# Kernel tuning notes

Measured on AMD Instinct MI355X. Metric: run time of the kernel, lower is better.

Reference implementation:

```python
import jax, jax.numpy as jnp
import numpy as np

# Pyramid configuration (mirrors InstancePyramid: init level grid + requested levels)
INIT_SIZE = (200, 200)
LEVEL_SIZES = [(200, 200), (100, 100), (50, 50), (25, 25), (13, 13)]
G = 28            # shared gaussian table side = feature_scale(7) * 4
CTR = 13          # table center index = 7*2 - 1
N_INST = 512


def _gaussian_table():
    # exp(-ln2 * ((x-13)^2 + (y-13)^2) / 7^2), identical to shared_gaussian_masks()
    xs = jnp.arange(G, dtype=jnp.float32)
    d2 = (xs - CTR) ** 2
    return jnp.exp(-jnp.log(jnp.float32(2.0)) * (d2[:, None] + d2[None, :]) / jnp.float32(7 ** 2))


def setup_inputs() -> dict:
    key = jax.random.key(0)
    pos = jax.random.randint(key, (N_INST, 2), 0, INIT_SIZE[0], dtype=jnp.int32)
    shared_mask = _gaussian_table()  # the fixed learnable-free 28x28 gaussian crop source
    return {"pos": pos, "shared_mask": shared_mask}


def _level_masks(shared_mask, pos, level_size):
    # Vectorized form of get_feature_gaussian_mask over all instances.
    H, W = level_size
    H0, W0 = INIT_SIZE
    # get_root_level_pos: round(pos / init_size * req_size)
    lh = jnp.round(pos[:, 0].astype(jnp.float32) / H0 * H).astype(jnp.int32)  # [N]
    lw = jnp.round(pos[:, 1].astype(jnp.float32) / W0 * W).astype(jnp.int32)  # [N]
    # feature pixel (x, y) reads shared_mask[CTR + x - lh, CTR + y - lw] when in [0, 28)
    si = CTR + jnp.arange(H, dtype=jnp.int32)[None, :] - lh[:, None]   # [N, H]
    sj = CTR + jnp.arange(W, dtype=jnp.int32)[None, :] - lw[:, None]   # [N, W]
    vi = (si >= 0) & (si < G)
    vj = (sj >= 0) & (sj < G)
    gi = jnp.clip(si, 0, G - 1)
    gj = jnp.clip(sj, 0, G - 1)
    m = shared_mask[gi[:, :, None], gj[:, None, :]]                    # [N, H, W] gather
    m = m * (vi[:, :, None] & vj[:, None, :]).astype(m.dtype)          # zero outside crop
    return m.reshape(m.shape[0], -1)


def reference(pos, shared_mask):
    # Per-instance gaussian heatmaps scattered into every pyramid level,
    # flattened and concatenated: [N, sum_l H_l*W_l] = [512, 53294]
    outs = [_level_masks(shared_mask, pos, ls) for ls in LEVEL_SIZES]
    return jnp.concatenate(outs, axis=1)
```

## Files before the change

### kernel.cpp

```cpp
#include <hip/hip_runtime.h>


#define G 28
#define CTR 13
#define ROW 53294
#define PAIRS 26647

template <int W, int BASE>
__device__ __forceinline__ float level_val(int r, int lh, int lw,
                                           const float* __restrict__ mask) {
  const int rr = r - BASE;
  const int i = rr / W;
  const int j = rr - i * W;
  const unsigned si = (unsigned)(CTR + i - lh);
  const unsigned sj = (unsigned)(CTR + j - lw);
  float v = 0.0f;
  if (si < (unsigned)G && sj < (unsigned)G) v = mask[si * G + sj];
  return v;
}

__global__ __launch_bounds__(256) void MaskPyramids_kernel(
    const int* __restrict__ pos, const float* __restrict__ mask,
    float* __restrict__ out) {
  const int inst = blockIdx.y;
  const int t = blockIdx.x * 256 + threadIdx.x;
  if (t >= PAIRS) return;

  const int p0 = pos[2 * inst];
  const int p1 = pos[2 * inst + 1];

  const float x0 = (float)p0 * 0.005f;
  const float x1 = (float)p1 * 0.005f;

  const int lh0 = (int)rintf(x0 * 200.0f), lw0 = (int)rintf(x1 * 200.0f);
  const int lh1 = (int)rintf(x0 * 100.0f), lw1 = (int)rintf(x1 * 100.0f);
  const int lh2 = (int)rintf(x0 * 50.0f),  lw2 = (int)rintf(x1 * 50.0f);
  const int lh3 = (int)rintf(x0 * 25.0f),  lw3 = (int)rintf(x1 * 25.0f);
  const int lh4 = (int)rintf(x0 * 13.0f),  lw4 = (int)rintf(x1 * 13.0f);

  const int r0 = 2 * t;
  float v[2];
#pragma unroll
  for (int u = 0; u < 2; ++u) {
    const int r = r0 + u;
    if (r < 40000)      v[u] = level_val<200, 0>(r, lh0, lw0, mask);
    else if (r < 50000) v[u] = level_val<100, 40000>(r, lh1, lw1, mask);
    else if (r < 52500) v[u] = level_val<50, 50000>(r, lh2, lw2, mask);
    else if (r < 53125) v[u] = level_val<25, 52500>(r, lh3, lw3, mask);
    else                v[u] = level_val<13, 53125>(r, lh4, lw4, mask);
  }

  float2* dst = (float2*)(out + (size_t)inst * ROW + r0);
  *dst = make_float2(v[0], v[1]);
}

extern "C" void kernel_launch(void* const* d_in, const int* in_sizes, int n_in,
                              void* d_out, int out_size, void* d_ws, size_t ws_size,
                              hipStream_t stream) {
  const int* pos = (const int*)d_in[0];
  const float* mask = (const float*)d_in[1];
  float* out = (float*)d_out;

  dim3 grid((PAIRS + 255) / 256, 512);
  MaskPyramids_kernel<<<grid, 256, 0, stream>>>(pos, mask, out);
}
```

Baseline: 137.9 us.

## Split into bulk float4 zero-fill plus sparse per-instance gaussian paint kernel

Replaces the per-element gather over the whole output with two kernels. The first writes zeros to the entire output with float4 stores. The second scatters only the 28x28 gaussian crop for each instance and level. This removes the per-element level dispatch, integer division and bounds tests from the bulk path, making it a pure store stream. In exchange it adds a second launch and a dependency between the two kernels, and the painted values are written after the zeros, so those locations are stored twice.

```diff
diff --git a/kernel.cpp b/kernel.cpp
--- a/kernel.cpp
+++ b/kernel.cpp
@@ -4,54 +4,52 @@
 #define G 28
 #define CTR 13
 #define ROW 53294
-#define PAIRS 26647
+#define TOTAL_F4 6821632
+#define FILL_BLOCKS 26647
 
-template <int W, int BASE>
-__device__ __forceinline__ float level_val(int r, int lh, int lw,
-                                           const float* __restrict__ mask) {
-  const int rr = r - BASE;
-  const int i = rr / W;
-  const int j = rr - i * W;
-  const unsigned si = (unsigned)(CTR + i - lh);
-  const unsigned sj = (unsigned)(CTR + j - lw);
-  float v = 0.0f;
-  if (si < (unsigned)G && sj < (unsigned)G) v = mask[si * G + sj];
-  return v;
+__global__ __launch_bounds__(256) void fill_zero_kernel(float4* __restrict__ out4) {
+  const int idx = blockIdx.x * 256 + threadIdx.x;
+  out4[idx] = make_float4(0.f, 0.f, 0.f, 0.f);
 }
 
-__global__ __launch_bounds__(256) void MaskPyramids_kernel(
+template <int H, int W, int BASE>
+__device__ __forceinline__ void paint(const float* __restrict__ mask,
+                                      float* __restrict__ row,
+                                      int lh, int lw) {
+  for (int c = threadIdx.x; c < G * G; c += 256) {
+    const int si = c / G;
+    const int sj = c - si * G;
+    const int i = lh + si - CTR;
+    const int j = lw + sj - CTR;
+    if ((unsigned)i < (unsigned)H && (unsigned)j < (unsigned)W)
+      row[BASE + i * W + j] = mask[c];
+  }
+}
+
+__global__ __launch_bounds__(256) void paint_kernel(
     const int* __restrict__ pos, const float* __restrict__ mask,
     float* __restrict__ out) {
-  const int inst = blockIdx.y;
-  const int t = blockIdx.x * 256 + threadIdx.x;
-  if (t >= PAIRS) return;
+  const int inst = blockIdx.x;
+  const int lvl  = blockIdx.y;
 
   const int p0 = pos[2 * inst];
   const int p1 = pos[2 * inst + 1];
-
   const float x0 = (float)p0 * 0.005f;
   const float x1 = (float)p1 * 0.005f;
 
-  const int lh0 = (int)rintf(x0 * 200.0f), lw0 = (int)rintf(x1 * 200.0f);
-  const int lh1 = (int)rintf(x0 * 100.0f), lw1 = (int)rintf(x1 * 100.0f);
-  const int lh2 = (int)rintf(x0 * 50.0f),  lw2 = (int)rintf(x1 * 50.0f);
-  const int lh3 = (int)rintf(x0 * 25.0f),  lw3 = (int)rintf(x1 * 25.0f);
-  const int lh4 = (int)rintf(x0 * 13.0f),  lw4 = (int)rintf(x1 * 13.0f);
-
-  const int r0 = 2 * t;
-  float v[2];
-#pragma unroll
-  for (int u = 0; u < 2; ++u) {
-    const int r = r0 + u;
-    if (r < 40000)      v[u] = level_val<200, 0>(r, lh0, lw0, mask);
-    else if (r < 50000) v[u] = level_val<100, 40000>(r, lh1, lw1, mask);
-    else if (r < 52500) v[u] = level_val<50, 50000>(r, lh2, lw2, mask);
-    else if (r < 53125) v[u] = level_val<25, 52500>(r, lh3, lw3, mask);
-    else                v[u] = level_val<13, 53125>(r, lh4, lw4, mask);
+  float* row = out + (size_t)inst * ROW;
+  switch (lvl) {
+    case 0: paint<200, 200, 0>(mask, row,
+              (int)rintf(x0 * 200.0f), (int)rintf(x1 * 200.0f)); break;
+    case 1: paint<100, 100, 40000>(mask, row,
+              (int)rintf(x0 * 100.0f), (int)rintf(x1 * 100.0f)); break;
+    case 2: paint<50, 50, 50000>(mask, row,
+              (int)rintf(x0 * 50.0f), (int)rintf(x1 * 50.0f)); break;
+    case 3: paint<25, 25, 52500>(mask, row,
+              (int)rintf(x0 * 25.0f), (int)rintf(x1 * 25.0f)); break;
+    default: paint<13, 13, 53125>(mask, row,
+              (int)rintf(x0 * 13.0f), (int)rintf(x1 * 13.0f)); break;
   }
-
-  float2* dst = (float2*)(out + (size_t)inst * ROW + r0);
-  *dst = make_float2(v[0], v[1]);
 }
 
 extern "C" void kernel_launch(void* const* d_in, const int* in_sizes, int n_in,
@@ -61,6 +59,7 @@
   const float* mask = (const float*)d_in[1];
   float* out = (float*)d_out;
 
-  dim3 grid((PAIRS + 255) / 256, 512);
-  MaskPyramids_kernel<<<grid, 256, 0, stream>>>(pos, mask, out);
+  fill_zero_kernel<<<FILL_BLOCKS, 256, 0, stream>>>((float4*)out);
+  dim3 pgrid(512, 5);
+  paint_kernel<<<pgrid, 256, 0, stream>>>(pos, mask, out);
 }
```

Measured after the change: 116.7 us. -15.3%, faster.
